# Optimization experiments

Hardware: AMD Instinct MI355X
Metric: run time of the kernel (lower is better)

The kernel has to match this reference:

```python
import jax, jax.numpy as jnp
from jax import lax
import numpy as np
import math

EPSILON = 0.05
ITER = 50
HALF_SIZE = 1
K = 2 * HALF_SIZE + 1          # 3
SIZE = K * K                   # 9, matches (2*half_size+1)**2
LOG_SIZE = math.log(SIZE)


def _smooth_trans(x, ker):
    # exp -> replicate pad -> 3x3 box-sum conv -> log -> scale (soft max-pool / dilation)
    e = jnp.exp(x / EPSILON)
    e = jnp.pad(e, ((0, 0), (0, 0), (1, 1), (1, 1)), mode='edge')
    s = lax.conv_general_dilated(
        e, ker, window_strides=(1, 1), padding='VALID',
        dimension_numbers=('NCHW', 'OIHW', 'NCHW'))
    return EPSILON * (jnp.log(s) - LOG_SIZE)


def setup_inputs() -> dict:
    key = jax.random.key(0)
    img = jax.random.uniform(key, (8, 1, 512, 512), dtype=jnp.float32)
    ker = jnp.ones((1, 1, K, K), dtype=jnp.float32)
    return {"img": img, "ker": ker}


def reference(img, ker):
    def erode(x):
        return -_smooth_trans(-x, ker)

    def dilate(x):
        return _smooth_trans(x, ker)

    def open_(x):
        return jnp.clip(dilate(erode(x)), 0.0, 1.0)

    skel = jax.nn.relu(img - open_(img))

    def step(carry, _):
        im, sk = carry
        im = erode(im)
        sk = sk + jax.nn.relu(im - open_(im))
        return (im, sk), None

    (_, skel), _ = lax.scan(step, (img, skel), None, length=ITER)
    return skel
```

## Files before the change

### kernel.cpp

```cpp
#include <hip/hip_runtime.h>

#define HH 512
#define WW 512
#define NB 8
#define TH 32
#define TW 64

__device__ __forceinline__ float rcp_f(float x)  { return __builtin_amdgcn_rcpf(x); }
__device__ __forceinline__ float log2_f(float x) { return __builtin_amdgcn_logf(x); }
__device__ __forceinline__ float exp2_f(float x) { return __builtin_amdgcn_exp2f(x); }

#define C1      0.034657359027997264f
#define LOG2_9  3.1699250014423126f
#define NEG_INV -28.853900817779268f

template<int A, bool LAST, bool E_IMG, bool WRITEU>
__device__ __forceinline__ void one_step(
    float* __restrict__ IN, float* __restrict__ OUT, float* __restrict__ H,
    int r0, int c0, int tid,
    float* __restrict__ uog, const float* __restrict__ imgb, float (&sk)[8])
{
    constexpr int SIN  = TW + 2*A;
    constexpr int RIN  = TH + 2*A;
    constexpr int B_   = A - 1;
    constexpr int SOUT = TW + 2*B_;
    constexpr int ROUT = TH + 2*B_;

    for (int i = tid; i < RIN*SOUT; i += 256) {
        int r = i / SOUT, c = i - r*SOUT;
        const float* p = IN + r*SIN + c;
        H[i] = p[0] + p[1] + p[2];
    }
    __syncthreads();

    for (int i = tid; i < ROUT*SOUT; i += 256) {
        int r = i / SOUT, c = i - r*SOUT;
        int gr = r0 - B_ + r, gc = c0 - B_ + c;
        int rcl = min(max(gr, 0), HH-1) - (r0 - B_);
        int ccl = min(max(gc, 0), WW-1) - (c0 - B_);
        const float* h = H + rcl*SOUT + ccl;
        float u1 = (h[0] + h[SOUT] + h[2*SOUT]) * (1.0f/9.0f);
        OUT[i] = u1;
        if constexpr (LAST && WRITEU) {
            if (r >= B_ && r < B_+TH && c >= B_ && c < B_+TW)
                uog[gr*WW + gc] = u1;
        }
    }
    __syncthreads();

    for (int i = tid; i < (TH+2)*TW; i += 256) {
        int r = i >> 6, c = i & (TW-1);
        const float* p = OUT + (B_-1+r)*SOUT + (B_-1+c);
        H[i] = rcp_f(p[0]) + rcp_f(p[1]) + rcp_f(p[2]);
    }
    __syncthreads();

    #pragma unroll
    for (int j = 0; j < 8; ++j) {
        int idx = j*256 + tid;
        int tr = idx >> 6, tc = idx & (TW-1);
        float sd = H[tr*TW+tc] + H[(tr+1)*TW+tc] + H[(tr+2)*TW+tc];
        float d = C1 * (log2_f(sd) - LOG2_9);
        d = fminf(fmaxf(d, 0.0f), 1.0f);
        float e;
        if constexpr (E_IMG) e = imgb[(r0+tr)*WW + (c0+tc)];
        else                 e = -C1 * log2_f(IN[(A+tr)*SIN + (A+tc)]);
        sk[j] += fmaxf(e - d, 0.0f);
    }
    __syncthreads();
}

template<int A, int REMAIN, bool E_IMG, bool WRITEU>
struct Chain {
    static __device__ __forceinline__ void run(
        float* IN, float* OUT, float* H, int r0, int c0, int tid,
        float* uog, const float* imgb, float (&sk)[8])
    {
        one_step<A, (REMAIN==1), E_IMG, WRITEU>(IN, OUT, H, r0, c0, tid, uog, imgb, sk);
        if constexpr (REMAIN > 1)
            Chain<A-1, REMAIN-1, false, WRITEU>::run(OUT, IN, H, r0, c0, tid, uog, imgb, sk);
    }
};

template<bool FIRST, int NSTEP, bool WRITEU>
__global__ __launch_bounds__(256)
void sk_fused(const float* __restrict__ u_in, const float* __restrict__ img,
              float* __restrict__ u_out, float* __restrict__ skel)
{
    constexpr int A0 = NSTEP + 1;
    constexpr int S0 = TW + 2*A0;
    constexpr int R0 = TH + 2*A0;
    __shared__ float bufA[(TH+12)*(TW+12)];
    __shared__ float bufB[(TH+12)*(TW+12)];
    __shared__ float bufH[(TH+12)*(TW+10)];

    const int b   = blockIdx.z;
    const int r0  = blockIdx.y * TH;
    const int c0  = blockIdx.x * TW;
    const int tid = threadIdx.x;
    const size_t boff = (size_t)b * (HH*WW);
    const float* imgb = img + boff;
    float* uog = u_out + boff;
    float* skb = skel + boff;

    for (int i = tid; i < R0*S0; i += 256) {
        int r = i / S0, c = i - r*S0;
        int gr = min(max(r0 - A0 + r, 0), HH-1);
        int gc = min(max(c0 - A0 + c, 0), WW-1);
        if constexpr (FIRST) bufA[i] = exp2_f(imgb[gr*WW+gc] * NEG_INV);
        else                 bufA[i] = (u_in + boff)[gr*WW+gc];
    }
    __syncthreads();

    float sk[8];
    #pragma unroll
    for (int j = 0; j < 8; ++j) sk[j] = 0.0f;

    Chain<A0, NSTEP, FIRST, WRITEU>::run(bufA, bufB, bufH, r0, c0, tid, uog, imgb, sk);

    #pragma unroll
    for (int j = 0; j < 8; ++j) {
        int idx = j*256 + tid;
        int tr = idx >> 6, tc = idx & (TW-1);
        float* sp = skb + (r0+tr)*WW + (c0+tc);
        if constexpr (FIRST) *sp = sk[j];
        else                 *sp += sk[j];
    }
}

extern "C" void kernel_launch(void* const* d_in, const int* in_sizes, int n_in,
                              void* d_out, int out_size, void* d_ws, size_t ws_size,
                              hipStream_t stream) {
    const float* img = (const float*)d_in[0];
    float* skel = (float*)d_out;
    const size_t N = (size_t)NB * HH * WW;
    float* ua = (float*)d_ws;
    float* ub = ua + N;

    dim3 grid(WW/TW, HH/TH, NB);

    sk_fused<true, 5, true><<<grid, 256, 0, stream>>>(nullptr, img, ua, skel);

    float* uin = ua; float* uout = ub;
    for (int t = 0; t < 9; ++t) {
        sk_fused<false, 5, true><<<grid, 256, 0, stream>>>(uin, img, uout, skel);
        float* tmp = uin; uin = uout; uout = tmp;
    }

    sk_fused<false, 1, false><<<grid, 256, 0, stream>>>(uin, img, uout, skel);
}
```

Measured before the change: 477.5 us.

## Vectorize stencil stages with float4 over fixed-stride shared tiles and two buffers

Reorganizes shared memory into two fixed-stride (80) padded tiles in place of three variable-stride buffers, and computes each separable 3-tap pass on float4 groups with neighbor scalars. The replicate-clamp path now runs only for border blocks, while interior blocks take a clamp-free vectorized path. Skeleton accumulation, the global loads of the image and skeleton, and the u writes move to float4. Launch bounds now request 5 blocks per CU. This cuts LDS instruction count, index arithmetic and shared footprint, at the cost of more complex indexing and divergent code for edge blocks.

```diff
diff --git a/kernel.cpp b/kernel.cpp
--- a/kernel.cpp
+++ b/kernel.cpp
@@ -5,6 +5,10 @@
 #define NB 8
 #define TH 32
 #define TW 64
+#define ST 80
+#define RB 48
+#define RO 8
+#define CO 8
 
 __device__ __forceinline__ float rcp_f(float x)  { return __builtin_amdgcn_rcpf(x); }
 __device__ __forceinline__ float log2_f(float x) { return __builtin_amdgcn_logf(x); }
@@ -14,117 +18,190 @@
 #define LOG2_9  3.1699250014423126f
 #define NEG_INV -28.853900817779268f
 
-template<int A, bool LAST, bool E_IMG, bool WRITEU>
+__device__ __forceinline__ float4 ld4(const float* p) { return *(const float4*)p; }
+__device__ __forceinline__ void   st4(float* p, float4 v) { *(float4*)p = v; }
+
+template<int B_, bool LAST, bool E_IMG, bool WRITEU>
 __device__ __forceinline__ void one_step(
-    float* __restrict__ IN, float* __restrict__ OUT, float* __restrict__ H,
-    int r0, int c0, int tid,
-    float* __restrict__ uog, const float* __restrict__ imgb, float (&sk)[8])
+    float* __restrict__ P, float* __restrict__ Q,
+    int r0, int c0, int tid, bool edge,
+    float* __restrict__ uog, const float* __restrict__ imgb,
+    float4 (&sk)[2])
 {
-    constexpr int SIN  = TW + 2*A;
-    constexpr int RIN  = TH + 2*A;
-    constexpr int B_   = A - 1;
-    constexpr int SOUT = TW + 2*B_;
-    constexpr int ROUT = TH + 2*B_;
-
-    for (int i = tid; i < RIN*SOUT; i += 256) {
-        int r = i / SOUT, c = i - r*SOUT;
-        const float* p = IN + r*SIN + c;
-        H[i] = p[0] + p[1] + p[2];
-    }
-    __syncthreads();
-
-    for (int i = tid; i < ROUT*SOUT; i += 256) {
-        int r = i / SOUT, c = i - r*SOUT;
-        int gr = r0 - B_ + r, gc = c0 - B_ + c;
-        int rcl = min(max(gr, 0), HH-1) - (r0 - B_);
-        int ccl = min(max(gc, 0), WW-1) - (c0 - B_);
-        const float* h = H + rcl*SOUT + ccl;
-        float u1 = (h[0] + h[SOUT] + h[2*SOUT]) * (1.0f/9.0f);
-        OUT[i] = u1;
-        if constexpr (LAST && WRITEU) {
-            if (r >= B_ && r < B_+TH && c >= B_ && c < B_+TW)
-                uog[gr*WW + gc] = u1;
-        }
-    }
-    __syncthreads();
-
-    for (int i = tid; i < (TH+2)*TW; i += 256) {
-        int r = i >> 6, c = i & (TW-1);
-        const float* p = OUT + (B_-1+r)*SOUT + (B_-1+c);
-        H[i] = rcp_f(p[0]) + rcp_f(p[1]) + rcp_f(p[2]);
+    constexpr int BC0 = (B_ == 5) ? 0 : 4;
+    constexpr int BCL = ((71 + B_) >> 2) << 2;
+    constexpr int NG  = (BCL - BC0) / 4 + 1;
+    constexpr int RA0 = RO - 1 - B_;
+    constexpr int NRA = TH + 2 + 2 * B_;
+    constexpr int RB0 = RO - B_;
+    constexpr int NRB = TH + 2 * B_;
+
+    float4 e[2];
+    if constexpr (!E_IMG) {
+        #pragma unroll
+        for (int j = 0; j < 2; ++j) {
+            int gi = j * 256 + tid;
+            int tr = RO + (gi >> 4), bc = CO + (gi & 15) * 4;
+            float4 u = ld4(P + tr * ST + bc);
+            e[j].x = -C1 * log2_f(u.x); e[j].y = -C1 * log2_f(u.y);
+            e[j].z = -C1 * log2_f(u.z); e[j].w = -C1 * log2_f(u.w);
+        }
+    }
+
+    for (int gi = tid; gi < NRA * NG; gi += 256) {
+        int rr = gi / NG;
+        int bc = BC0 + (gi - rr * NG) * 4;
+        const float* row = P + (RA0 + rr) * ST;
+        float4 q = ld4(row + bc);
+        float pm1 = row[bc > 0 ? bc - 1 : 0];
+        float p4  = row[bc + 4];
+        float4 o;
+        o.x = pm1 + q.x + q.y; o.y = q.x + q.y + q.z;
+        o.z = q.y + q.z + q.w; o.w = q.z + q.w + p4;
+        st4(Q + (RA0 + rr) * ST + bc, o);
+    }
+    __syncthreads();
+
+    if (!edge) {
+        for (int gi = tid; gi < NRB * NG; gi += 256) {
+            int rr = gi / NG;
+            int bc = BC0 + (gi - rr * NG) * 4;
+            int r = RB0 + rr;
+            const float* h = Q + (r - 1) * ST + bc;
+            float4 t = ld4(h), m = ld4(h + ST), b = ld4(h + 2 * ST);
+            float4 u;
+            u.x = (t.x + m.x + b.x) * (1.0f / 9.0f);
+            u.y = (t.y + m.y + b.y) * (1.0f / 9.0f);
+            u.z = (t.z + m.z + b.z) * (1.0f / 9.0f);
+            u.w = (t.w + m.w + b.w) * (1.0f / 9.0f);
+            st4(P + r * ST + bc, u);
+            if constexpr (LAST && WRITEU) {
+                if (r >= RO && r < RO + TH && bc >= CO && bc < CO + TW)
+                    *(float4*)(uog + (size_t)(r0 + r - RO) * WW + (c0 + bc - CO)) = u;
+            }
+        }
+    } else {
+        constexpr int WID = TW + 2 * B_;
+        for (int i = tid; i < NRB * WID; i += 256) {
+            int rr = i / WID;
+            int c  = (CO - B_) + (i - rr * WID);
+            int r  = RB0 + rr;
+            int gr = r0 + r - RO, gc = c0 + c - CO;
+            int rcl = min(max(gr, 0), HH - 1) - r0 + RO;
+            int ccl = min(max(gc, 0), WW - 1) - c0 + CO;
+            float u = (Q[(rcl - 1) * ST + ccl] + Q[rcl * ST + ccl] + Q[(rcl + 1) * ST + ccl]) * (1.0f / 9.0f);
+            P[r * ST + c] = u;
+            if constexpr (LAST && WRITEU) {
+                if (r >= RO && r < RO + TH && c >= CO && c < CO + TW)
+                    uog[(size_t)gr * WW + gc] = u;
+            }
+        }
+    }
+    __syncthreads();
+
+    for (int gi = tid; gi < (TH + 2) * 16; gi += 256) {
+        int rr = gi >> 4;
+        int bc = CO + (gi & 15) * 4;
+        const float* row = P + (RO - 1 + rr) * ST;
+        float4 q = ld4(row + bc);
+        float pm1 = row[bc - 1], p4 = row[bc + 4];
+        float a0 = rcp_f(pm1), a1 = rcp_f(q.x), a2 = rcp_f(q.y),
+              a3 = rcp_f(q.z), a4 = rcp_f(q.w), a5 = rcp_f(p4);
+        float4 o;
+        o.x = a0 + a1 + a2; o.y = a1 + a2 + a3;
+        o.z = a2 + a3 + a4; o.w = a3 + a4 + a5;
+        st4(Q + (RO - 1 + rr) * ST + bc, o);
     }
     __syncthreads();
 
     #pragma unroll
-    for (int j = 0; j < 8; ++j) {
-        int idx = j*256 + tid;
-        int tr = idx >> 6, tc = idx & (TW-1);
-        float sd = H[tr*TW+tc] + H[(tr+1)*TW+tc] + H[(tr+2)*TW+tc];
-        float d = C1 * (log2_f(sd) - LOG2_9);
-        d = fminf(fmaxf(d, 0.0f), 1.0f);
-        float e;
-        if constexpr (E_IMG) e = imgb[(r0+tr)*WW + (c0+tc)];
-        else                 e = -C1 * log2_f(IN[(A+tr)*SIN + (A+tc)]);
-        sk[j] += fmaxf(e - d, 0.0f);
+    for (int j = 0; j < 2; ++j) {
+        int gi = j * 256 + tid;
+        int tr = RO + (gi >> 4), bc = CO + (gi & 15) * 4;
+        const float* h = Q + (tr - 1) * ST + bc;
+        float4 t = ld4(h), m = ld4(h + ST), b = ld4(h + 2 * ST);
+        float4 d;
+        d.x = fminf(fmaxf(C1 * (log2_f(t.x + m.x + b.x) - LOG2_9), 0.0f), 1.0f);
+        d.y = fminf(fmaxf(C1 * (log2_f(t.y + m.y + b.y) - LOG2_9), 0.0f), 1.0f);
+        d.z = fminf(fmaxf(C1 * (log2_f(t.z + m.z + b.z) - LOG2_9), 0.0f), 1.0f);
+        d.w = fminf(fmaxf(C1 * (log2_f(t.w + m.w + b.w) - LOG2_9), 0.0f), 1.0f);
+        float4 ee;
+        if constexpr (E_IMG)
+            ee = *(const float4*)(imgb + (size_t)(r0 + tr - RO) * WW + (c0 + bc - CO));
+        else
+            ee = e[j];
+        sk[j].x += fmaxf(ee.x - d.x, 0.0f);
+        sk[j].y += fmaxf(ee.y - d.y, 0.0f);
+        sk[j].z += fmaxf(ee.z - d.z, 0.0f);
+        sk[j].w += fmaxf(ee.w - d.w, 0.0f);
     }
     __syncthreads();
 }
 
-template<int A, int REMAIN, bool E_IMG, bool WRITEU>
+template<int B_, int REMAIN, bool E_IMG, bool WRITEU>
 struct Chain {
     static __device__ __forceinline__ void run(
-        float* IN, float* OUT, float* H, int r0, int c0, int tid,
-        float* uog, const float* imgb, float (&sk)[8])
+        float* P, float* Q, int r0, int c0, int tid, bool edge,
+        float* uog, const float* imgb, float4 (&sk)[2])
     {
-        one_step<A, (REMAIN==1), E_IMG, WRITEU>(IN, OUT, H, r0, c0, tid, uog, imgb, sk);
+        one_step<B_, (REMAIN == 1), E_IMG, WRITEU>(P, Q, r0, c0, tid, edge, uog, imgb, sk);
         if constexpr (REMAIN > 1)
-            Chain<A-1, REMAIN-1, false, WRITEU>::run(OUT, IN, H, r0, c0, tid, uog, imgb, sk);
+            Chain<B_ - 1, REMAIN - 1, false, WRITEU>::run(P, Q, r0, c0, tid, edge, uog, imgb, sk);
     }
 };
 
 template<bool FIRST, int NSTEP, bool WRITEU>
-__global__ __launch_bounds__(256)
+__global__ __launch_bounds__(256, 5)
 void sk_fused(const float* __restrict__ u_in, const float* __restrict__ img,
               float* __restrict__ u_out, float* __restrict__ skel)
 {
     constexpr int A0 = NSTEP + 1;
-    constexpr int S0 = TW + 2*A0;
-    constexpr int R0 = TH + 2*A0;
-    __shared__ float bufA[(TH+12)*(TW+12)];
-    __shared__ float bufB[(TH+12)*(TW+12)];
-    __shared__ float bufH[(TH+12)*(TW+10)];
-
-    const int b   = blockIdx.z;
+    __shared__ __align__(16) float P[RB * ST];
+    __shared__ __align__(16) float Q[RB * ST];
+
     const int r0  = blockIdx.y * TH;
     const int c0  = blockIdx.x * TW;
     const int tid = threadIdx.x;
-    const size_t boff = (size_t)b * (HH*WW);
+    const bool edge = (blockIdx.x == 0) | (blockIdx.x == gridDim.x - 1) |
+                      (blockIdx.y == 0) | (blockIdx.y == gridDim.y - 1);
+    const size_t boff = (size_t)blockIdx.z * (HH * WW);
     const float* imgb = img + boff;
     float* uog = u_out + boff;
     float* skb = skel + boff;
 
-    for (int i = tid; i < R0*S0; i += 256) {
-        int r = i / S0, c = i - r*S0;
-        int gr = min(max(r0 - A0 + r, 0), HH-1);
-        int gc = min(max(c0 - A0 + c, 0), WW-1);
-        if constexpr (FIRST) bufA[i] = exp2_f(imgb[gr*WW+gc] * NEG_INV);
-        else                 bufA[i] = (u_in + boff)[gr*WW+gc];
-    }
-    __syncthreads();
-
-    float sk[8];
+    {
+        constexpr int SH = TH + 2 * A0, SW = TW + 2 * A0;
+        const float* uin = u_in + boff;
+        for (int i = tid; i < SH * SW; i += 256) {
+            int rr = i / SW, cc = i - rr * SW;
+            int gr = min(max(r0 + rr - A0, 0), HH - 1);
+            int gc = min(max(c0 + cc - A0, 0), WW - 1);
+            float v;
+            if constexpr (FIRST) v = exp2_f(imgb[gr * WW + gc] * NEG_INV);
+            else                 v = uin[gr * WW + gc];
+            P[(RO - A0 + rr) * ST + (CO - A0 + cc)] = v;
+        }
+    }
+    __syncthreads();
+
+    float4 sk[2];
+    sk[0] = make_float4(0.f, 0.f, 0.f, 0.f);
+    sk[1] = make_float4(0.f, 0.f, 0.f, 0.f);
+
+    Chain<NSTEP, NSTEP, FIRST, WRITEU>::run(P, Q, r0, c0, tid, edge, uog, imgb, sk);
+
     #pragma unroll
-    for (int j = 0; j < 8; ++j) sk[j] = 0.0f;
-
-    Chain<A0, NSTEP, FIRST, WRITEU>::run(bufA, bufB, bufH, r0, c0, tid, uog, imgb, sk);
-
-    #pragma unroll
-    for (int j = 0; j < 8; ++j) {
-        int idx = j*256 + tid;
-        int tr = idx >> 6, tc = idx & (TW-1);
-        float* sp = skb + (r0+tr)*WW + (c0+tc);
-        if constexpr (FIRST) *sp = sk[j];
-        else                 *sp += sk[j];
+    for (int j = 0; j < 2; ++j) {
+        int gi = j * 256 + tid;
+        int tr = RO + (gi >> 4), bc = CO + (gi & 15) * 4;
+        float* sp = skb + (size_t)(r0 + tr - RO) * WW + (c0 + bc - CO);
+        if constexpr (FIRST) {
+            *(float4*)sp = sk[j];
+        } else {
+            float4 old = *(const float4*)sp;
+            old.x += sk[j].x; old.y += sk[j].y; old.z += sk[j].z; old.w += sk[j].w;
+            *(float4*)sp = old;
+        }
     }
 }
 
@@ -137,7 +214,7 @@
     float* ua = (float*)d_ws;
     float* ub = ua + N;
 
-    dim3 grid(WW/TW, HH/TH, NB);
+    dim3 grid(WW / TW, HH / TH, NB);
 
     sk_fused<true, 5, true><<<grid, 256, 0, stream>>>(nullptr, img, ua, skel);
 
```

Result: faster. 423.0 us (-11.4%).
